# Optimization experiments

Hardware: AMD Instinct MI355X
Metric: run time of the kernel (lower is better)

## Reference

```python
import jax, jax.numpy as jnp
import numpy as np

ALPHA = 1.0
DIAG_FILL = 500000.0


def _batch_pairwise_dist(x, y):
    # x: [B, Nx, D], y: [B, Ny, D] -> squared-distance matrix [B, Nx, Ny]
    xx = jnp.sum(x * x, axis=-1)  # [B, Nx]
    yy = jnp.sum(y * y, axis=-1)  # [B, Ny]
    zz = jnp.einsum('bnd,bmd->bnm', x, y)  # [B, Nx, Ny]
    return xx[:, :, None] + yy[:, None, :] - 2.0 * zz


def setup_inputs() -> dict:
    key = jax.random.key(0)
    k1, k2 = jax.random.split(key)
    B, N, D = 4, 4096, 3
    gts = jax.random.normal(k1, (B, N, D), dtype=jnp.float32)
    preds = jax.random.normal(k2, (B, N, D), dtype=jnp.float32)
    return {"gts": gts, "preds": preds}


def reference(gts, preds):
    # Cross-term Chamfer: P[b,i,j] = ||gts_i - preds_j||^2
    P = _batch_pairwise_dist(gts, preds)  # [B, Ng, Np]
    loss_1 = jnp.sum(jnp.min(P, axis=1), axis=1)  # min over gts, sum over preds
    loss_2 = jnp.sum(jnp.min(P, axis=2), axis=1)  # min over preds, sum over gts

    # Self nearest-neighbor distance distributions (diagonal masked out)
    Ng = gts.shape[1]
    Np = preds.shape[1]
    eye_g = jnp.eye(Ng, dtype=bool)
    eye_p = jnp.eye(Np, dtype=bool)
    P1 = jnp.where(eye_g[None, :, :], DIAG_FILL, _batch_pairwise_dist(gts, gts))
    P2 = jnp.where(eye_p[None, :, :], DIAG_FILL, _batch_pairwise_dist(preds, preds))

    mins1 = jnp.sort(jnp.min(P1, axis=1), axis=1)  # [B, Ng]
    mins2 = jnp.sort(jnp.min(P2, axis=1), axis=1)  # [B, Np]
    min_ps = min(mins1.shape[1], mins2.shape[1])
    loss_ordering = jnp.sum((mins1[:, :min_ps] - mins2[:, :min_ps]) ** 2, axis=1)

    return loss_1 + loss_2 + ALPHA * loss_ordering
```

## Files before the change

### kernel.cpp

```cpp
#include <hip/hip_runtime.h>

constexpr int BATCH = 4;
constexpr int NPTS  = 4096;
constexpr int QC    = 1024;
constexpr int TC    = 512;
constexpr int NTHR  = 256;
constexpr int QPT   = QC / NTHR;


__global__ __launch_bounds__(256) void nn_init(unsigned int* __restrict__ m) {
    int i = blockIdx.x * blockDim.x + threadIdx.x;
    m[i] = 0x7F800000u;
}

__global__ __launch_bounds__(NTHR) void nn_pass(const float* __restrict__ gts,
                                                const float* __restrict__ preds,
                                                unsigned int* __restrict__ nnmin) {
    const int pass  = blockIdx.z & 3;
    const int b     = blockIdx.z >> 2;
    const int qbase = blockIdx.y * QC;
    const int tbase = blockIdx.x * TC;
    const bool selfp = (pass >= 2);
    const float* __restrict__ A = (pass == 0 || pass == 2) ? gts : preds;
    const float* __restrict__ T = (pass == 1 || pass == 2) ? gts : preds;

    __shared__ float4 tp[TC];
    for (int k = threadIdx.x; k < TC; k += NTHR) {
        const float* p = T + ((size_t)b * NPTS + tbase + k) * 3;
        tp[k] = make_float4(p[0], p[1], p[2], 0.f);
    }
    __syncthreads();

    float qx[QPT], qy[QPT], qz[QPT], mn[QPT];
    int qidx[QPT];
#pragma unroll
    for (int q = 0; q < QPT; ++q) {
        const int qi = qbase + threadIdx.x + q * NTHR;
        qidx[q] = qi;
        const float* p = A + ((size_t)b * NPTS + qi) * 3;
        qx[q] = p[0]; qy[q] = p[1]; qz[q] = p[2];
        mn[q] = 1e30f;
    }

    if (selfp) {
#pragma unroll 4
        for (int j = 0; j < TC; ++j) {
            const float4 t = tp[j];
            const int tj = tbase + j;
#pragma unroll
            for (int q = 0; q < QPT; ++q) {
                const float dx = qx[q] - t.x, dy = qy[q] - t.y, dz = qz[q] - t.z;
                float d = dx * dx;
                d = fmaf(dy, dy, d);
                d = fmaf(dz, dz, d);
                d = (tj == qidx[q]) ? 1e30f : d;
                mn[q] = fminf(mn[q], d);
            }
        }
    } else {
#pragma unroll 4
        for (int j = 0; j < TC; ++j) {
            const float4 t = tp[j];
#pragma unroll
            for (int q = 0; q < QPT; ++q) {
                const float dx = qx[q] - t.x, dy = qy[q] - t.y, dz = qz[q] - t.z;
                float d = dx * dx;
                d = fmaf(dy, dy, d);
                d = fmaf(dz, dz, d);
                mn[q] = fminf(mn[q], d);
            }
        }
    }

    unsigned int* dst = nnmin + ((size_t)pass * BATCH + b) * NPTS;
#pragma unroll
    for (int q = 0; q < QPT; ++q)
        atomicMin(&dst[qidx[q]], __float_as_uint(mn[q]));
}

__global__ __launch_bounds__(1024) void nn_sort(unsigned int* __restrict__ nnmin) {
    const int which = blockIdx.x & 1;
    const int b     = blockIdx.x >> 1;
    unsigned int* src = nnmin + ((size_t)(2 + which) * BATCH + b) * NPTS;
    __shared__ float s[NPTS];
    for (int i = threadIdx.x; i < NPTS; i += 1024) s[i] = __uint_as_float(src[i]);

    for (int k = 2; k <= NPTS; k <<= 1) {
        for (int j = k >> 1; j > 0; j >>= 1) {
            __syncthreads();
#pragma unroll
            for (int t = threadIdx.x; t < NPTS / 2; t += 1024) {
                const int i = ((t & ~(j - 1)) << 1) | (t & (j - 1));
                const int p = i | j;
                const bool up = ((i & k) == 0);
                const float a = s[i], c = s[p];
                if ((a > c) == up) { s[i] = c; s[p] = a; }
            }
        }
    }
    __syncthreads();
    for (int i = threadIdx.x; i < NPTS; i += 1024) src[i] = __float_as_uint(s[i]);
}

__global__ __launch_bounds__(512) void nn_reduce(const unsigned int* __restrict__ nnmin,
                                                 float* __restrict__ out) {
    const int b = blockIdx.x;
    const int tid = threadIdx.x;
    __shared__ float red[512];

    const unsigned int* m0 = nnmin + ((size_t)0 * BATCH + b) * NPTS;
    const unsigned int* m1 = nnmin + ((size_t)1 * BATCH + b) * NPTS;
    const unsigned int* s1 = nnmin + ((size_t)2 * BATCH + b) * NPTS;
    const unsigned int* s2 = nnmin + ((size_t)3 * BATCH + b) * NPTS;

    float acc = 0.f;
    for (int i = tid; i < NPTS; i += 512) {
        acc += __uint_as_float(m0[i]) + __uint_as_float(m1[i]);
        const float d = __uint_as_float(s1[i]) - __uint_as_float(s2[i]);
        acc = fmaf(d, d, acc);
    }

    red[tid] = acc;
    __syncthreads();
    for (int s = 256; s > 0; s >>= 1) {
        if (tid < s) red[tid] += red[tid + s];
        __syncthreads();
    }
    if (tid == 0) out[b] = red[0];
}

extern "C" void kernel_launch(void* const* d_in, const int* in_sizes, int n_in,
                              void* d_out, int out_size, void* d_ws, size_t ws_size,
                              hipStream_t stream) {
    const float* gts   = (const float*)d_in[0];
    const float* preds = (const float*)d_in[1];
    float* out = (float*)d_out;
    unsigned int* nnmin = (unsigned int*)d_ws;

    nn_init<<<(4 * BATCH * NPTS) / 256, 256, 0, stream>>>(nnmin);
    dim3 grid(NPTS / TC, NPTS / QC, BATCH * 4);
    nn_pass<<<grid, NTHR, 0, stream>>>(gts, preds, nnmin);
    nn_sort<<<2 * BATCH, 1024, 0, stream>>>(nnmin);
    nn_reduce<<<BATCH, 512, 0, stream>>>(nnmin, out);
}
```

Baseline: 132.9 us.

## Use symmetric 2D tiles with row/column minima and register-shuffle bitonic sort

The distance pass now uses 128x128 tiles that compute each pairwise distance once and update both the row minima and the column minima. That halves the cross work (gts-to-preds and preds-to-gts share one tile) and exploits symmetry in the self passes with upper-triangular tiles. The sort keeps 4 elements per thread in registers and uses wave shuffles for strides below 256, touching shared memory only for large strides. The trade-off is more atomics per tile, shared-memory reductions of the partial minima, and a serial loop to map each block to its triangular tile.

New measurement: 125.9 us. 5.2% less time.

```diff
diff --git a/kernel.cpp b/kernel.cpp
--- a/kernel.cpp
+++ b/kernel.cpp
@@ -2,10 +2,11 @@
 
 constexpr int BATCH = 4;
 constexpr int NPTS  = 4096;
-constexpr int QC    = 1024;
-constexpr int TC    = 512;
-constexpr int NTHR  = 256;
-constexpr int QPT   = QC / NTHR;
+constexpr int TILE  = 128;
+constexpr int NT    = NPTS / TILE;
+constexpr int CROSS_TILES = NT * NT;
+constexpr int TRI_TILES   = NT * (NT + 1) / 2;
+constexpr int TILES_PER_BATCH = CROSS_TILES + 2 * TRI_TILES;
 
 
 __global__ __launch_bounds__(256) void nn_init(unsigned int* __restrict__ m) {
@@ -13,93 +14,163 @@
     m[i] = 0x7F800000u;
 }
 
-__global__ __launch_bounds__(NTHR) void nn_pass(const float* __restrict__ gts,
-                                                const float* __restrict__ preds,
-                                                unsigned int* __restrict__ nnmin) {
-    const int pass  = blockIdx.z & 3;
-    const int b     = blockIdx.z >> 2;
-    const int qbase = blockIdx.y * QC;
-    const int tbase = blockIdx.x * TC;
-    const bool selfp = (pass >= 2);
-    const float* __restrict__ A = (pass == 0 || pass == 2) ? gts : preds;
-    const float* __restrict__ T = (pass == 1 || pass == 2) ? gts : preds;
-
-    __shared__ float4 tp[TC];
-    for (int k = threadIdx.x; k < TC; k += NTHR) {
-        const float* p = T + ((size_t)b * NPTS + tbase + k) * 3;
-        tp[k] = make_float4(p[0], p[1], p[2], 0.f);
+__global__ __launch_bounds__(256) void nn_pass(const float* __restrict__ gts,
+                                               const float* __restrict__ preds,
+                                               unsigned int* __restrict__ nnmin) {
+    const int b = blockIdx.y;
+    int id = blockIdx.x;
+    const float* A; const float* Bp;
+    unsigned int* rowslot; unsigned int* colslot;
+    int I, J;
+    bool self;
+    if (id < CROSS_TILES) {
+        A = gts; Bp = preds;
+        I = id >> 5; J = id & 31;
+        rowslot = nnmin + ((size_t)0 * BATCH + b) * NPTS;
+        colslot = nnmin + ((size_t)1 * BATCH + b) * NPTS;
+        self = false;
+    } else {
+        id -= CROSS_TILES;
+        const int which = id / TRI_TILES;
+        int t = id - which * TRI_TILES;
+        int i = 0;
+        while (t >= NT - i) { t -= NT - i; ++i; }
+        I = i; J = i + t;
+        A = which ? preds : gts; Bp = A;
+        rowslot = colslot = nnmin + ((size_t)(2 + which) * BATCH + b) * NPTS;
+        self = true;
+    }
+
+    __shared__ float4 arow[TILE];
+    __shared__ float4 bcol[TILE];
+    __shared__ float  rp[TILE][17];
+    __shared__ float  cp[TILE][17];
+
+    const int tid = threadIdx.x;
+    if (tid < TILE) {
+        const float* p = A + ((size_t)b * NPTS + I * TILE + tid) * 3;
+        arow[tid] = make_float4(p[0], p[1], p[2], 0.f);
+    } else {
+        const float* p = Bp + ((size_t)b * NPTS + J * TILE + (tid - TILE)) * 3;
+        bcol[tid - TILE] = make_float4(p[0], p[1], p[2], 0.f);
     }
     __syncthreads();
 
-    float qx[QPT], qy[QPT], qz[QPT], mn[QPT];
-    int qidx[QPT];
-#pragma unroll
-    for (int q = 0; q < QPT; ++q) {
-        const int qi = qbase + threadIdx.x + q * NTHR;
-        qidx[q] = qi;
-        const float* p = A + ((size_t)b * NPTS + qi) * 3;
-        qx[q] = p[0]; qy[q] = p[1]; qz[q] = p[2];
-        mn[q] = 1e30f;
-    }
-
-    if (selfp) {
-#pragma unroll 4
-        for (int j = 0; j < TC; ++j) {
-            const float4 t = tp[j];
-            const int tj = tbase + j;
-#pragma unroll
-            for (int q = 0; q < QPT; ++q) {
-                const float dx = qx[q] - t.x, dy = qy[q] - t.y, dz = qz[q] - t.z;
-                float d = dx * dx;
-                d = fmaf(dy, dy, d);
-                d = fmaf(dz, dz, d);
-                d = (tj == qidx[q]) ? 1e30f : d;
-                mn[q] = fminf(mn[q], d);
-            }
-        }
+    const int tx = tid & 15, ty = tid >> 4;
+    float ax[8], ay[8], az[8], bx[8], by[8], bz[8];
+#pragma unroll
+    for (int r = 0; r < 8; ++r) {
+        const float4 t = arow[ty * 8 + r];
+        ax[r] = t.x; ay[r] = t.y; az[r] = t.z;
+    }
+#pragma unroll
+    for (int c = 0; c < 8; ++c) {
+        const float4 t = bcol[tx * 8 + c];
+        bx[c] = t.x; by[c] = t.y; bz[c] = t.z;
+    }
+
+    float rmin[8], cmin[8];
+#pragma unroll
+    for (int r = 0; r < 8; ++r) { rmin[r] = 1e30f; cmin[r] = 1e30f; }
+
+    const bool dt = self && (I == J) && (ty == tx);
+
+#pragma unroll
+    for (int r = 0; r < 8; ++r) {
+#pragma unroll
+        for (int c = 0; c < 8; ++c) {
+            const float dx = ax[r] - bx[c];
+            const float dy = ay[r] - by[c];
+            const float dz = az[r] - bz[c];
+            float d = fmaf(dz, dz, fmaf(dy, dy, dx * dx));
+            if (r == c) d = dt ? 1e30f : d;
+            rmin[r] = fminf(rmin[r], d);
+            cmin[c] = fminf(cmin[c], d);
+        }
+    }
+
+#pragma unroll
+    for (int r = 0; r < 8; ++r) rp[ty * 8 + r][tx] = rmin[r];
+#pragma unroll
+    for (int c = 0; c < 8; ++c) cp[tx * 8 + c][ty] = cmin[c];
+    __syncthreads();
+
+    if (tid < TILE) {
+        float m = rp[tid][0];
+#pragma unroll
+        for (int i = 1; i < 16; ++i) m = fminf(m, rp[tid][i]);
+        atomicMin(&rowslot[I * TILE + tid], __float_as_uint(m));
     } else {
-#pragma unroll 4
-        for (int j = 0; j < TC; ++j) {
-            const float4 t = tp[j];
-#pragma unroll
-            for (int q = 0; q < QPT; ++q) {
-                const float dx = qx[q] - t.x, dy = qy[q] - t.y, dz = qz[q] - t.z;
-                float d = dx * dx;
-                d = fmaf(dy, dy, d);
-                d = fmaf(dz, dz, d);
-                mn[q] = fminf(mn[q], d);
-            }
-        }
-    }
-
-    unsigned int* dst = nnmin + ((size_t)pass * BATCH + b) * NPTS;
-#pragma unroll
-    for (int q = 0; q < QPT; ++q)
-        atomicMin(&dst[qidx[q]], __float_as_uint(mn[q]));
+        const int t2 = tid - TILE;
+        float m = cp[t2][0];
+#pragma unroll
+        for (int i = 1; i < 16; ++i) m = fminf(m, cp[t2][i]);
+        atomicMin(&colslot[J * TILE + t2], __float_as_uint(m));
+    }
 }
 
 __global__ __launch_bounds__(1024) void nn_sort(unsigned int* __restrict__ nnmin) {
     const int which = blockIdx.x & 1;
-    const int b     = blockIdx.x >> 1;
+    const int b = blockIdx.x >> 1;
     unsigned int* src = nnmin + ((size_t)(2 + which) * BATCH + b) * NPTS;
     __shared__ float s[NPTS];
-    for (int i = threadIdx.x; i < NPTS; i += 1024) s[i] = __uint_as_float(src[i]);
+    const int tid = threadIdx.x;
+    const int base = tid * 4;
+
+    const uint4 u = reinterpret_cast<const uint4*>(src)[tid];
+    float v[4] = {__uint_as_float(u.x), __uint_as_float(u.y),
+                  __uint_as_float(u.z), __uint_as_float(u.w)};
 
     for (int k = 2; k <= NPTS; k <<= 1) {
-        for (int j = k >> 1; j > 0; j >>= 1) {
+        if (k >= 512) {
+            s[base + 0] = v[0]; s[base + 1] = v[1]; s[base + 2] = v[2]; s[base + 3] = v[3];
             __syncthreads();
-#pragma unroll
-            for (int t = threadIdx.x; t < NPTS / 2; t += 1024) {
-                const int i = ((t & ~(j - 1)) << 1) | (t & (j - 1));
-                const int p = i | j;
-                const bool up = ((i & k) == 0);
-                const float a = s[i], c = s[p];
-                if ((a > c) == up) { s[i] = c; s[p] = a; }
+            for (int j = k >> 1; j >= 256; j >>= 1) {
+#pragma unroll
+                for (int tt = 0; tt < 2; ++tt) {
+                    const int t = tid + tt * 1024;
+                    const int i = ((t & ~(j - 1)) << 1) | (t & (j - 1));
+                    const int p = i | j;
+                    const bool asc = ((i & k) == 0);
+                    const float a = s[i], c = s[p];
+                    const float lo = fminf(a, c), hi = fmaxf(a, c);
+                    s[i] = asc ? lo : hi;
+                    s[p] = asc ? hi : lo;
+                }
+                __syncthreads();
             }
-        }
-    }
-    __syncthreads();
-    for (int i = threadIdx.x; i < NPTS; i += 1024) src[i] = __float_as_uint(s[i]);
+            v[0] = s[base + 0]; v[1] = s[base + 1]; v[2] = s[base + 2]; v[3] = s[base + 3];
+        }
+        for (int j = (k >> 1) > 128 ? 128 : (k >> 1); j >= 4; j >>= 1) {
+            const int m = j >> 2;
+#pragma unroll
+            for (int e = 0; e < 4; ++e) {
+                const float p = __shfl_xor(v[e], m, 64);
+                const int i = base + e;
+                const bool keepmin = (((i & j) == 0) == ((i & k) == 0));
+                v[e] = keepmin ? fminf(v[e], p) : fmaxf(v[e], p);
+            }
+        }
+        if (k >= 4) {
+            const bool asc2 = ((base & k) == 0);
+            float lo = fminf(v[0], v[2]), hi = fmaxf(v[0], v[2]);
+            v[0] = asc2 ? lo : hi; v[2] = asc2 ? hi : lo;
+            lo = fminf(v[1], v[3]); hi = fmaxf(v[1], v[3]);
+            v[1] = asc2 ? lo : hi; v[3] = asc2 ? hi : lo;
+        }
+        {
+            const bool ascA = (((base + 0) & k) == 0);
+            const bool ascB = (((base + 2) & k) == 0);
+            float lo = fminf(v[0], v[1]), hi = fmaxf(v[0], v[1]);
+            v[0] = ascA ? lo : hi; v[1] = ascA ? hi : lo;
+            lo = fminf(v[2], v[3]); hi = fmaxf(v[2], v[3]);
+            v[2] = ascB ? lo : hi; v[3] = ascB ? hi : lo;
+        }
+    }
+
+    reinterpret_cast<uint4*>(src)[tid] =
+        make_uint4(__float_as_uint(v[0]), __float_as_uint(v[1]),
+                   __float_as_uint(v[2]), __float_as_uint(v[3]));
 }
 
 __global__ __launch_bounds__(512) void nn_reduce(const unsigned int* __restrict__ nnmin,
@@ -138,8 +209,8 @@
     unsigned int* nnmin = (unsigned int*)d_ws;
 
     nn_init<<<(4 * BATCH * NPTS) / 256, 256, 0, stream>>>(nnmin);
-    dim3 grid(NPTS / TC, NPTS / QC, BATCH * 4);
-    nn_pass<<<grid, NTHR, 0, stream>>>(gts, preds, nnmin);
+    dim3 grid(TILES_PER_BATCH, BATCH);
+    nn_pass<<<grid, 256, 0, stream>>>(gts, preds, nnmin);
     nn_sort<<<2 * BATCH, 1024, 0, stream>>>(nnmin);
     nn_reduce<<<BATCH, 512, 0, stream>>>(nnmin, out);
 }
```
